# Kernel optimization log

Measured on AMD Instinct MI355X. Metric: run time of the kernel, lower is better.

The kernel has to match this reference:

```python
import jax, jax.numpy as jnp
import numpy as np

B, H, W, Z = 2, 256, 256, 256


def _shift_zero(x, axis, offset):
    """Shift x along `axis` by `offset`, zero-filling the vacated slab.
    offset=-1: out[i] = x[i-1]; offset=+1: out[i] = x[i+1]."""
    pad = [(0, 0)] * x.ndim
    idx = [slice(None)] * x.ndim
    if offset == -1:
        pad[axis] = (1, 0)
        idx[axis] = slice(0, x.shape[axis])
    else:
        pad[axis] = (0, 1)
        idx[axis] = slice(1, x.shape[axis] + 1)
    return jnp.pad(x, pad)[tuple(idx)]


def apply_7pt_stencil(x, coeff):
    # x: [B,H,W,Z], coeff: [B,H,W,7] broadcast over Z
    west = _shift_zero(x, 2, -1)
    east = _shift_zero(x, 2, 1)
    south = _shift_zero(x, 1, -1)
    north = _shift_zero(x, 1, 1)
    bottom = _shift_zero(x, 3, -1)
    top = _shift_zero(x, 3, 1)
    c = coeff[..., None, :]  # [B,H,W,1,7]
    return (c[..., 0] * west + c[..., 1] * east + c[..., 2] * south
            + c[..., 3] * north + c[..., 4] * bottom + c[..., 5] * top
            + c[..., 6] * x)


def setup_inputs() -> dict:
    key = jax.random.key(0)
    k1, k2, k3 = jax.random.split(key, 3)
    x = jax.random.normal(k1, (B, H, W, Z), dtype=jnp.float32)
    coeff = jax.random.uniform(k2, (B, H, W, 7), dtype=jnp.float32)
    ref = jax.random.normal(k3, (B, H, W, Z), dtype=jnp.float32)
    return {"x": x, "coeff": coeff, "ref": ref}


def reference(x, coeff, ref):
    output = apply_7pt_stencil(x, coeff)
    error = (output - ref).astype(jnp.float32)
    loss = jnp.mean(error * error)
    max_abs_error = jnp.max(jnp.abs(error))
    return loss, output, max_abs_error
```

## Files before the change

### kernel.cpp

```cpp
#include <hip/hip_runtime.h>

#define BB 2
#define HH 256
#define WW 256
#define ZZ 256
#define NROWS (BB * HH * WW)
#define NELEM ((long long)NROWS * ZZ)

#define NBLK 2048
#define WPB 4
#define TOT_WAVES (NBLK * WPB)
#define ROWS_PER_WAVE (NROWS / TOT_WAVES)

typedef float vf4 __attribute__((ext_vector_type(4)));

__device__ __forceinline__ float4 ld4(const float* p) { return *(const float4*)p; }

__global__ __launch_bounds__(256) void stencil7_kernel(
    const float* __restrict__ x, const float* __restrict__ coeff,
    const float* __restrict__ ref, float* __restrict__ outD,
    float* __restrict__ part_sum, float* __restrict__ part_max)
{
    const int tid  = threadIdx.x;
    const int wave = tid >> 6;
    const int lane = tid & 63;
    const int waveId = blockIdx.x * WPB + wave;
    const int z0   = lane << 2;

    float acc_s = 0.f;
    float acc_m = 0.f;

    #pragma unroll 1
    for (int it = 0; it < ROWS_PER_WAVE; ++it) {
        const int r = waveId + it * TOT_WAVES;
        const int w = r & (WW - 1);
        const int h = (r >> 8) & (HH - 1);
        const long long base = (long long)r * ZZ;

        const float4 cen = ld4(x + base + z0);
        float4 west  = make_float4(0.f, 0.f, 0.f, 0.f);
        float4 east  = west, south = west, north = west;
        if (w > 0)      west  = ld4(x + base - ZZ + z0);
        if (w < WW - 1) east  = ld4(x + base + ZZ + z0);
        if (h > 0)      south = ld4(x + base - (long long)WW * ZZ + z0);
        if (h < HH - 1) north = ld4(x + base + (long long)WW * ZZ + z0);
        const float4 rf = ld4(ref + base + z0);

        const float* cp = coeff + 7LL * __builtin_amdgcn_readfirstlane(r);
        const float c0 = cp[0], c1 = cp[1], c2 = cp[2], c3 = cp[3];
        const float c4 = cp[4], c5 = cp[5], c6 = cp[6];

        float bm1 = __shfl_up(cen.w, 1);
        if (lane == 0) bm1 = 0.f;
        float tp1 = __shfl_down(cen.x, 1);
        if (lane == 63) tp1 = 0.f;

        const float4 bot = make_float4(bm1, cen.x, cen.y, cen.z);
        const float4 top = make_float4(cen.y, cen.z, cen.w, tp1);

        float4 o;
        o.x = c0*west.x + c1*east.x + c2*south.x + c3*north.x + c4*bot.x + c5*top.x + c6*cen.x;
        o.y = c0*west.y + c1*east.y + c2*south.y + c3*north.y + c4*bot.y + c5*top.y + c6*cen.y;
        o.z = c0*west.z + c1*east.z + c2*south.z + c3*north.z + c4*bot.z + c5*top.z + c6*cen.z;
        o.w = c0*west.w + c1*east.w + c2*south.w + c3*north.w + c4*bot.w + c5*top.w + c6*cen.w;

        const float nx = __shfl_down(o.x, 1);
        const float ny = __shfl_down(o.y, 1);
        const float nz = __shfl_down(o.z, 1);
        float* rowp = outD + base;
        if (lane < 63) {
            vf4 st; st.x = o.w; st.y = nx; st.z = ny; st.w = nz;
            __builtin_nontemporal_store(st, (vf4*)(rowp + 4 * (lane + 1)));
        }
        if (lane == 0) { rowp[1] = o.x; rowp[2] = o.y; rowp[3] = o.z; }
        if (lane == 63) rowp[ZZ] = o.w;

        const float ex = o.x - rf.x, ey = o.y - rf.y, ez = o.z - rf.z, ew = o.w - rf.w;
        acc_s += ex*ex + ey*ey + ez*ez + ew*ew;
        acc_m  = fmaxf(acc_m, fmaxf(fmaxf(fabsf(ex), fabsf(ey)),
                                    fmaxf(fabsf(ez), fabsf(ew))));
    }

    #pragma unroll
    for (int off = 32; off > 0; off >>= 1) {
        acc_s += __shfl_down(acc_s, off);
        acc_m  = fmaxf(acc_m, __shfl_down(acc_m, off));
    }

    __shared__ float ss[WPB];
    __shared__ float sm[WPB];
    if (lane == 0) { ss[wave] = acc_s; sm[wave] = acc_m; }
    __syncthreads();
    if (tid == 0) {
        part_sum[blockIdx.x] = ss[0] + ss[1] + ss[2] + ss[3];
        part_max[blockIdx.x] = fmaxf(fmaxf(sm[0], sm[1]), fmaxf(sm[2], sm[3]));
    }
}

__global__ __launch_bounds__(256) void finalize_kernel(
    const float* __restrict__ part_sum, const float* __restrict__ part_max,
    float* __restrict__ loss_out, float* __restrict__ amax_out)
{
    const int tid  = threadIdx.x;
    const int wave = tid >> 6;
    const int lane = tid & 63;

    double s = 0.0;
    float  m = 0.f;
    for (int i = tid; i < NBLK; i += 256) {
        s += (double)part_sum[i];
        m  = fmaxf(m, part_max[i]);
    }
    #pragma unroll
    for (int off = 32; off > 0; off >>= 1) {
        s += __shfl_down(s, off);
        m  = fmaxf(m, __shfl_down(m, off));
    }
    __shared__ double ds[4];
    __shared__ float  dm[4];
    if (lane == 0) { ds[wave] = s; dm[wave] = m; }
    __syncthreads();
    if (tid == 0) {
        const double S = ds[0] + ds[1] + ds[2] + ds[3];
        const float  M = fmaxf(fmaxf(dm[0], dm[1]), fmaxf(dm[2], dm[3]));
        *loss_out = (float)(S / (double)NELEM);
        *amax_out = M;
    }
}

extern "C" void kernel_launch(void* const* d_in, const int* in_sizes, int n_in,
                              void* d_out, int out_size, void* d_ws, size_t ws_size,
                              hipStream_t stream) {
    const float* x     = (const float*)d_in[0];
    const float* coeff = (const float*)d_in[1];
    const float* ref   = (const float*)d_in[2];

    float* outf = (float*)d_out;
    float* loss_out = outf;
    float* amax_out = outf + 1 + NELEM;

    float* part_sum = (float*)d_ws;
    float* part_max = part_sum + NBLK;

    stencil7_kernel<<<dim3(NBLK), dim3(256), 0, stream>>>(
        x, coeff, ref, outf, part_sum, part_max);
    finalize_kernel<<<dim3(1), dim3(256), 0, stream>>>(
        part_sum, part_max, loss_out, amax_out);
}
```

Before: 92.26 us.

## Walk contiguous 16-row segments per wave with register rolling of west/center/east rows

Each wave now processes a contiguous segment of 16 consecutive W-rows rather than rows strided across the grid. The west/center/east rows rotate through registers, so each x row is loaded about once per segment instead of three times, and next-row loads are software-pipelined ahead of the compute. Blocks are remapped so that each XCD handles a contiguous range of segments for L2 locality. Loads of ref are marked nontemporal. The changes raise register pressure from full unrolling, and the grid now has 2048 blocks with 16 rows per wave.

```diff
diff --git a/kernel.cpp b/kernel.cpp
--- a/kernel.cpp
+++ b/kernel.cpp
@@ -7,14 +7,18 @@
 #define NROWS (BB * HH * WW)
 #define NELEM ((long long)NROWS * ZZ)
 
-#define NBLK 2048
+#define SEGROWS 16
+#define NSEG (NROWS / SEGROWS)
 #define WPB 4
-#define TOT_WAVES (NBLK * WPB)
-#define ROWS_PER_WAVE (NROWS / TOT_WAVES)
+#define NBLK (NSEG / WPB)
+#define NXCD 8
 
 typedef float vf4 __attribute__((ext_vector_type(4)));
 
-__device__ __forceinline__ float4 ld4(const float* p) { return *(const float4*)p; }
+__device__ __forceinline__ vf4 ld4(const float* p) { return *(const vf4*)p; }
+__device__ __forceinline__ vf4 ldnt4(const float* p) {
+    return __builtin_nontemporal_load((const vf4*)p);
+}
 
 __global__ __launch_bounds__(256) void stencil7_kernel(
     const float* __restrict__ x, const float* __restrict__ coeff,
@@ -22,63 +26,121 @@
     float* __restrict__ part_sum, float* __restrict__ part_max)
 {
     const int tid  = threadIdx.x;
-    const int wave = tid >> 6;
+    const int k    = tid >> 6;
     const int lane = tid & 63;
-    const int waveId = blockIdx.x * WPB + wave;
-    const int z0   = lane << 2;
-
-    float acc_s = 0.f;
-    float acc_m = 0.f;
-
-    #pragma unroll 1
-    for (int it = 0; it < ROWS_PER_WAVE; ++it) {
-        const int r = waveId + it * TOT_WAVES;
-        const int w = r & (WW - 1);
-        const int h = (r >> 8) & (HH - 1);
-        const long long base = (long long)r * ZZ;
-
-        const float4 cen = ld4(x + base + z0);
-        float4 west  = make_float4(0.f, 0.f, 0.f, 0.f);
-        float4 east  = west, south = west, north = west;
-        if (w > 0)      west  = ld4(x + base - ZZ + z0);
-        if (w < WW - 1) east  = ld4(x + base + ZZ + z0);
-        if (h > 0)      south = ld4(x + base - (long long)WW * ZZ + z0);
-        if (h < HH - 1) north = ld4(x + base + (long long)WW * ZZ + z0);
-        const float4 rf = ld4(ref + base + z0);
-
-        const float* cp = coeff + 7LL * __builtin_amdgcn_readfirstlane(r);
-        const float c0 = cp[0], c1 = cp[1], c2 = cp[2], c3 = cp[3];
-        const float c4 = cp[4], c5 = cp[5], c6 = cp[6];
-
-        float bm1 = __shfl_up(cen.w, 1);
+    const int b    = blockIdx.x;
+    const int sb   = (b & (NXCD - 1)) * (NBLK / NXCD) + (b >> 3);
+    const int seg  = sb * WPB + k;
+    const int r0   = __builtin_amdgcn_readfirstlane(seg * SEGROWS);
+    const int w0   = r0 & (WW - 1);
+    const int bh   = r0 >> 8;
+    const int h    = bh & (HH - 1);
+    const bool hasS = (h > 0);
+    const bool hasN = (h < HH - 1);
+    const long long SOFF = hasS ? -(long long)(WW * ZZ) : 0;
+    const long long NOFF = hasN ?  (long long)(WW * ZZ) : 0;
+    const int lo = lane << 2;
+
+    const float* px  = x   + (long long)r0 * ZZ + lo;
+    const float* prf = ref + (long long)r0 * ZZ + lo;
+    const float* pc  = coeff + 7LL * r0;
+    float* prow = outD + (long long)r0 * ZZ;
+
+    const vf4 z4 = {0.f, 0.f, 0.f, 0.f};
+
+    vf4 cw  = ld4(px + ((w0 > 0) ? -ZZ : 0));
+    vf4 cc  = ld4(px);
+    vf4 ce  = ld4(px + ZZ);
+    vf4 s_c = ld4(px + SOFF);
+    vf4 n_c = ld4(px + NOFF);
+    vf4 rf  = ldnt4(prf);
+    float k0 = pc[0], k1 = pc[1], k2 = pc[2], k3 = pc[3],
+          k4 = pc[4], k5 = pc[5], k6 = pc[6];
+    if (w0 == 0) cw = z4;
+
+    float acc_s = 0.f, acc_m = 0.f;
+
+    #pragma unroll
+    for (int i = 0; i < SEGROWS - 1; ++i) {
+        long long coff = (long long)(i + 2) * ZZ;
+        if (r0 + i + 2 >= NROWS) coff = (long long)(i + 1) * ZZ;
+        vf4 cnx = ld4(px + coff);
+        vf4 s_n = ld4(px + (long long)(i + 1) * ZZ + SOFF);
+        vf4 n_n = ld4(px + (long long)(i + 1) * ZZ + NOFF);
+        vf4 rfn = ldnt4(prf + (long long)(i + 1) * ZZ);
+        const float* pcn = pc + 7 * (i + 1);
+        const float d0 = pcn[0], d1 = pcn[1], d2 = pcn[2], d3 = pcn[3],
+                    d4 = pcn[4], d5 = pcn[5], d6 = pcn[6];
+
+        const vf4 sv = hasS ? s_c : z4;
+        const vf4 nv = hasN ? n_c : z4;
+        float bm1 = __shfl_up(cc.w, 1);
         if (lane == 0) bm1 = 0.f;
-        float tp1 = __shfl_down(cen.x, 1);
+        float tp1 = __shfl_down(cc.x, 1);
         if (lane == 63) tp1 = 0.f;
-
-        const float4 bot = make_float4(bm1, cen.x, cen.y, cen.z);
-        const float4 top = make_float4(cen.y, cen.z, cen.w, tp1);
-
-        float4 o;
-        o.x = c0*west.x + c1*east.x + c2*south.x + c3*north.x + c4*bot.x + c5*top.x + c6*cen.x;
-        o.y = c0*west.y + c1*east.y + c2*south.y + c3*north.y + c4*bot.y + c5*top.y + c6*cen.y;
-        o.z = c0*west.z + c1*east.z + c2*south.z + c3*north.z + c4*bot.z + c5*top.z + c6*cen.z;
-        o.w = c0*west.w + c1*east.w + c2*south.w + c3*north.w + c4*bot.w + c5*top.w + c6*cen.w;
+        const vf4 bot = {bm1, cc.x, cc.y, cc.z};
+        const vf4 top = {cc.y, cc.z, cc.w, tp1};
+
+        const vf4 o = k0*cw + k1*ce + k2*sv + k3*nv + k4*bot + k5*top + k6*cc;
 
         const float nx = __shfl_down(o.x, 1);
         const float ny = __shfl_down(o.y, 1);
         const float nz = __shfl_down(o.z, 1);
-        float* rowp = outD + base;
+        float* rowp = prow + (long long)i * ZZ;
         if (lane < 63) {
-            vf4 st; st.x = o.w; st.y = nx; st.z = ny; st.w = nz;
+            vf4 st = {o.w, nx, ny, nz};
             __builtin_nontemporal_store(st, (vf4*)(rowp + 4 * (lane + 1)));
         }
-        if (lane == 0) { rowp[1] = o.x; rowp[2] = o.y; rowp[3] = o.z; }
-        if (lane == 63) rowp[ZZ] = o.w;
-
-        const float ex = o.x - rf.x, ey = o.y - rf.y, ez = o.z - rf.z, ew = o.w - rf.w;
-        acc_s += ex*ex + ey*ey + ez*ez + ew*ew;
-        acc_m  = fmaxf(acc_m, fmaxf(fmaxf(fabsf(ex), fabsf(ey)),
-                                    fmaxf(fabsf(ez), fabsf(ew))));
+        if (lane == 0) {
+            __builtin_nontemporal_store(o.x, rowp + 1);
+            __builtin_nontemporal_store(o.y, rowp + 2);
+            __builtin_nontemporal_store(o.z, rowp + 3);
+        }
+        if (lane == 63) __builtin_nontemporal_store(o.w, rowp + ZZ);
+
+        const vf4 e = o - rf;
+        acc_s += e.x*e.x + e.y*e.y + e.z*e.z + e.w*e.w;
+        acc_m  = fmaxf(acc_m, fmaxf(fmaxf(fabsf(e.x), fabsf(e.y)),
+                                    fmaxf(fabsf(e.z), fabsf(e.w))));
+
+        cw = cc; cc = ce; ce = cnx;
+        s_c = s_n; n_c = n_n; rf = rfn;
+        k0 = d0; k1 = d1; k2 = d2; k3 = d3; k4 = d4; k5 = d5; k6 = d6;
+    }
+
+    {
+        const int i = SEGROWS - 1;
+        const vf4 ev = (w0 + i == WW - 1) ? z4 : ce;
+        const vf4 sv = hasS ? s_c : z4;
+        const vf4 nv = hasN ? n_c : z4;
+        float bm1 = __shfl_up(cc.w, 1);
+        if (lane == 0) bm1 = 0.f;
+        float tp1 = __shfl_down(cc.x, 1);
+        if (lane == 63) tp1 = 0.f;
+        const vf4 bot = {bm1, cc.x, cc.y, cc.z};
+        const vf4 top = {cc.y, cc.z, cc.w, tp1};
+
+        const vf4 o = k0*cw + k1*ev + k2*sv + k3*nv + k4*bot + k5*top + k6*cc;
+
+        const float nx = __shfl_down(o.x, 1);
+        const float ny = __shfl_down(o.y, 1);
+        const float nz = __shfl_down(o.z, 1);
+        float* rowp = prow + (long long)i * ZZ;
+        if (lane < 63) {
+            vf4 st = {o.w, nx, ny, nz};
+            __builtin_nontemporal_store(st, (vf4*)(rowp + 4 * (lane + 1)));
+        }
+        if (lane == 0) {
+            __builtin_nontemporal_store(o.x, rowp + 1);
+            __builtin_nontemporal_store(o.y, rowp + 2);
+            __builtin_nontemporal_store(o.z, rowp + 3);
+        }
+        if (lane == 63) __builtin_nontemporal_store(o.w, rowp + ZZ);
+
+        const vf4 e = o - rf;
+        acc_s += e.x*e.x + e.y*e.y + e.z*e.z + e.w*e.w;
+        acc_m  = fmaxf(acc_m, fmaxf(fmaxf(fabsf(e.x), fabsf(e.y)),
+                                    fmaxf(fabsf(e.z), fabsf(e.w))));
     }
 
     #pragma unroll
@@ -86,10 +148,9 @@
         acc_s += __shfl_down(acc_s, off);
         acc_m  = fmaxf(acc_m, __shfl_down(acc_m, off));
     }
-
     __shared__ float ss[WPB];
     __shared__ float sm[WPB];
-    if (lane == 0) { ss[wave] = acc_s; sm[wave] = acc_m; }
+    if (lane == 0) { ss[k] = acc_s; sm[k] = acc_m; }
     __syncthreads();
     if (tid == 0) {
         part_sum[blockIdx.x] = ss[0] + ss[1] + ss[2] + ss[3];
```

New measurement: 97.55 us. 5.7% more time.
